# Kernel tuning notes

Measured on AMD Instinct MI355X. Metric: run time of the kernel, lower is better.

The kernel has to match this reference:

```python
import jax, jax.numpy as jnp
import numpy as np

HADAMARD_DIM = 4096  # power of 2 -> had_rem_dim is None, rem_dim = 1


def _fwht(x):
    """Fast Walsh-Hadamard transform along last dim (natural/Sylvester order).

    x: [B, n] with n a power of 2. Returns x @ H_n (unnormalized).
    Mirrors QuaRot's recursive butterfly: at each stage, pairs are split into
    (a+b) and (a-b) halves. log2(n) stages, each O(n) work per row.
    """
    bsz, n = x.shape
    steps = int(np.log2(n))
    u = x[:, :, None]  # [B, n, 1]
    m = n
    for _ in range(steps):  # fixed-trip loop over log2(n) stages, jit-friendly
        u = u.reshape(bsz, m // 2, 2, -1)
        a = u[:, :, 0, :]
        b = u[:, :, 1, :]
        u = jnp.concatenate([a + b, a - b], axis=-1)  # [B, m//2, 2k]
        m //= 2
    return u.reshape(bsz, n)


def matmul_hadU(x):
    """QuaRot matmul_hadU for power-of-2 dim: normalized FWHT, 1/sqrt(n)."""
    n = x.shape[-1]
    flat = x.reshape(-1, n)
    out = _fwht(flat) * (1.0 / np.sqrt(n))
    return out.reshape(x.shape).astype(x.dtype)


def setup_inputs() -> dict:
    key = jax.random.key(0)
    x = jax.random.normal(key, (8192, HADAMARD_DIM), dtype=jnp.float32)
    return {"x": x}


def reference(x):
    # FWHT.forward: x -> matmul_hadU_cuda(x, None, 1) -> cast back to x.dtype
    return matmul_hadU(x)
```

## Files before the change

kernel.cpp:

```cpp
#include <hip/hip_runtime.h>


#define N        4096
#define THREADS  256
#define A_STR    20
#define B_STR    328
#define LDS_FLOATS (B_STR * 15 + A_STR * 15 + 16)

__device__ __forceinline__ void fwht16(float v[16]) {
#pragma unroll
    for (int s = 1; s < 16; s <<= 1) {
#pragma unroll
        for (int k = 0; k < 16; k++) {
            if ((k & s) == 0) {
                float a = v[k];
                float b = v[k + s];
                v[k]     = a + b;
                v[k + s] = a - b;
            }
        }
    }
}

__global__ __launch_bounds__(THREADS)
void FWHT_83476984365427_kernel(const float* __restrict__ x,
                                float* __restrict__ out,
                                int nrows) {
    __shared__ float lds[LDS_FLOATS];

    const int row = blockIdx.x;
    if (row >= nrows) return;

    const float* __restrict__ xr  = x   + (size_t)row * N;
    float* __restrict__       otr = out + (size_t)row * N;
    const int t = threadIdx.x;

    float v[16];

    {
        const float4* xv = (const float4*)xr + (size_t)t * 4;
#pragma unroll
        for (int c = 0; c < 4; c++) {
            float4 f = xv[c];
            v[4 * c + 0] = f.x;
            v[4 * c + 1] = f.y;
            v[4 * c + 2] = f.z;
            v[4 * c + 3] = f.w;
        }
    }
    fwht16(v);

    {
        const int i2 = t >> 4;
        const int i1 = t & 15;
        float* dst = &lds[A_STR * i1 + B_STR * i2];
#pragma unroll
        for (int c = 0; c < 4; c++) {
            float4 f;
            f.x = v[4 * c + 0];
            f.y = v[4 * c + 1];
            f.z = v[4 * c + 2];
            f.w = v[4 * c + 3];
            *(float4*)(dst + 4 * c) = f;
        }
    }
    __syncthreads();

    {
        const int i2 = t >> 4;
        const int i0 = t & 15;
        const int base = i0 + B_STR * i2;
#pragma unroll
        for (int k = 0; k < 16; k++) v[k] = lds[base + A_STR * k];
        fwht16(v);
#pragma unroll
        for (int k = 0; k < 16; k++) lds[base + A_STR * k] = v[k];
    }
    __syncthreads();

    {
        const int i1 = t >> 4;
        const int i0 = t & 15;
        const int base = i0 + A_STR * i1;
#pragma unroll
        for (int k = 0; k < 16; k++) v[k] = lds[base + B_STR * k];
        fwht16(v);
        const float scale = 1.0f / 64.0f;
#pragma unroll
        for (int k = 0; k < 16; k++) otr[k * 256 + t] = v[k] * scale;
    }
}

extern "C" void kernel_launch(void* const* d_in, const int* in_sizes, int n_in,
                              void* d_out, int out_size, void* d_ws, size_t ws_size,
                              hipStream_t stream) {
    (void)n_in; (void)d_ws; (void)ws_size; (void)out_size;
    const float* x = (const float*)d_in[0];
    float* out = (float*)d_out;
    const int nrows = in_sizes[0] / N;
    dim3 grid(nrows);
    dim3 block(THREADS);
    FWHT_83476984365427_kernel<<<grid, block, 0, stream>>>(x, out, nrows);
}
```

Before: 226.3 us.

## Coalesce global loads via strided float4 indexing and restructure LDS index decomposition

Global loads now have each thread read float4s strided by 256, so adjacent lanes touch adjacent addresses, instead of each thread reading 64 contiguous bytes. The FWHT index space is redecomposed into four dimensions with new LDS strides (4, 76, 1204), so each of the three radix-16 stages maps to a different layout while avoiding bank conflicts. The output write order changes to match, and stores use nontemporal hints to avoid polluting the cache. The risk is mis-mapping the butterfly dimensions and unexpected LDS bank conflicts with the new strides.

```diff
diff --git a/kernel.cpp b/kernel.cpp
--- a/kernel.cpp
+++ b/kernel.cpp
@@ -3,9 +3,10 @@
 
 #define N        4096
 #define THREADS  256
-#define A_STR    20
-#define B_STR    328
-#define LDS_FLOATS (B_STR * 15 + A_STR * 15 + 16)
+#define D1 4
+#define D2 76
+#define D3 1204
+#define LDS_FLOATS (3 + D1*15 + D2*15 + D3*3 + 1)
 
 __device__ __forceinline__ void fwht16(float v[16]) {
 #pragma unroll
@@ -38,10 +39,10 @@
     float v[16];
 
     {
-        const float4* xv = (const float4*)xr + (size_t)t * 4;
+        const float4* xv = (const float4*)xr;
 #pragma unroll
         for (int c = 0; c < 4; c++) {
-            float4 f = xv[c];
+            float4 f = xv[c * 256 + t];
             v[4 * c + 0] = f.x;
             v[4 * c + 1] = f.y;
             v[4 * c + 2] = f.z;
@@ -51,9 +52,9 @@
     fwht16(v);
 
     {
-        const int i2 = t >> 4;
-        const int i1 = t & 15;
-        float* dst = &lds[A_STR * i1 + B_STR * i2];
+        const int d1 = t & 15;
+        const int d2 = t >> 4;
+        float* dst = &lds[D1 * d1 + D2 * d2];
 #pragma unroll
         for (int c = 0; c < 4; c++) {
             float4 f;
@@ -61,33 +62,38 @@
             f.y = v[4 * c + 1];
             f.z = v[4 * c + 2];
             f.w = v[4 * c + 3];
-            *(float4*)(dst + 4 * c) = f;
+            *(float4*)(dst + D3 * c) = f;
         }
     }
     __syncthreads();
 
     {
-        const int i2 = t >> 4;
-        const int i0 = t & 15;
-        const int base = i0 + B_STR * i2;
+        const int d0 = t & 3;
+        const int d2 = (t >> 2) & 15;
+        const int d3 = t >> 6;
+        const int base = d0 + D2 * d2 + D3 * d3;
 #pragma unroll
-        for (int k = 0; k < 16; k++) v[k] = lds[base + A_STR * k];
+        for (int k = 0; k < 16; k++) v[k] = lds[base + D1 * k];
         fwht16(v);
 #pragma unroll
-        for (int k = 0; k < 16; k++) lds[base + A_STR * k] = v[k];
+        for (int k = 0; k < 16; k++) lds[base + D1 * k] = v[k];
     }
     __syncthreads();
 
     {
-        const int i1 = t >> 4;
-        const int i0 = t & 15;
-        const int base = i0 + A_STR * i1;
+        const int d0 = t & 3;
+        const int d1 = (t >> 2) & 15;
+        const int d3 = t >> 6;
+        const int base = d0 + D1 * d1 + D3 * d3;
 #pragma unroll
-        for (int k = 0; k < 16; k++) v[k] = lds[base + B_STR * k];
+        for (int k = 0; k < 16; k++) v[k] = lds[base + D2 * k];
         fwht16(v);
         const float scale = 1.0f / 64.0f;
+        const int eb = (t & 63) + 1024 * (t >> 6);
 #pragma unroll
-        for (int k = 0; k < 16; k++) otr[k * 256 + t] = v[k] * scale;
+        for (int k = 0; k < 16; k++) {
+            __builtin_nontemporal_store(v[k] * scale, &otr[64 * k + eb]);
+        }
     }
 }
 
```

Result: no change. 229.1 us (+1.2%).
